# Performance work log

Measured on AMD Instinct MI355X. Metric: run time of the kernel, lower is better.

## Reference

```python
import jax, jax.numpy as jnp
import numpy as np

# ---- Haar DWT (levels=1, mode='zero'), matches pytorch_wavelets ordering ----
# For even H,W and filter length 2, zero-pad haar analysis reduces to
# non-overlapping 2x2 blocks. Subband order after the two 1D analyses
# (width first, then height): LL, (w-lo,h-hi), (w-hi,h-lo), HH.

def haar_dwt(x):
    a = x[..., 0::2, 0::2]
    b = x[..., 0::2, 1::2]
    c = x[..., 1::2, 0::2]
    d = x[..., 1::2, 1::2]
    ll = (a + b + c + d) * 0.5
    h0 = (a + b - c - d) * 0.5   # lo-width, hi-height
    h1 = (a - b + c - d) * 0.5   # hi-width, lo-height
    hh = (a - b - c + d) * 0.5
    return ll, jnp.stack([h0, h1, hh], axis=2)  # yh: (b,c,3,h/2,w/2)


def _interleave(u, v, axis):
    # interleave two equal-shaped arrays along `axis` (negative axis)
    s = list(u.shape)
    s[axis] *= 2
    return jnp.stack([u, v], axis=axis + len(u.shape) + 1).reshape(s)


def haar_idwt(ll, yh):
    h0, h1, hh = yh[:, :, 0], yh[:, :, 1], yh[:, :, 2]
    a = (ll + h0 + h1 + hh) * 0.5
    b = (ll + h0 - h1 - hh) * 0.5
    c = (ll - h0 + h1 - hh) * 0.5
    d = (ll - h0 - h1 + hh) * 0.5
    top = _interleave(a, b, -1)   # even rows
    bot = _interleave(c, d, -1)   # odd rows
    return _interleave(top, bot, -2)


def batched_dynamic_conv(feat, kernels, pad):
    """feat: (b,cin,h,w), kernels: (b,cout,cin,kh,kw) -> (b,cout,h,w).
    Per-sample kernels via grouped conv (batch as groups)."""
    bsz, cin, h, w = feat.shape
    cout, kh, kw = kernels.shape[1], kernels.shape[3], kernels.shape[4]
    lhs = feat.reshape(1, bsz * cin, h, w)
    rhs = kernels.reshape(bsz * cout, cin, kh, kw)
    out = jax.lax.conv_general_dilated(
        lhs, rhs, window_strides=(1, 1), padding=[(pad, pad), (pad, pad)],
        dimension_numbers=('NCHW', 'OIHW', 'NCHW'), feature_group_count=bsz)
    return out.reshape(bsz, cout, h, w)


def _dyn_conv_subband(feat, sub_kernels, attn_w, attn_b, pad=1):
    # attention: 1x1 conv -> global avg pool -> softmax over kernel_num
    logits = jnp.einsum('bchw,kc->bk', feat, attn_w) / (feat.shape[-2] * feat.shape[-1]) + attn_b
    att = jax.nn.softmax(logits, axis=1)                       # (b,K)
    kernels = jnp.einsum('bk,koiuv->boiuv', att, sub_kernels)  # (b,cout,cin,kh,kw)
    return batched_dynamic_conv(feat, kernels, pad)


def setup_inputs() -> dict:
    key = jax.random.key(0)
    k1, k2, k3, k4 = jax.random.split(key, 4)
    B, C, H, W = 8, 64, 128, 128
    K, SUB, COUT, KS = 4, 4, 64, 3  # kernel_num, 1+3*levels, out_channels, kernel_size
    return {
        'x': jax.random.normal(k1, (B, C, H, W), dtype=jnp.float32),
        'wt_kernels': jax.random.normal(k2, (K, SUB, COUT, C, KS, KS), dtype=jnp.float32) * 0.02,
        'attn_w': jax.random.normal(k3, (K, C), dtype=jnp.float32) * 0.1,
        'attn_b': jnp.zeros((K,), dtype=jnp.float32),
    }


def reference(x, wt_kernels, attn_w, attn_b):
    ll, yh = haar_dwt(x)
    subbands = [ll, yh[:, :, 0], yh[:, :, 1], yh[:, :, 2]]
    outs = [_dyn_conv_subband(sb, wt_kernels[:, i], attn_w, attn_b, pad=1)
            for i, sb in enumerate(subbands)]
    rec_yh = jnp.stack(outs[1:4], axis=2)  # (b,cout,3,h/2,w/2)
    return haar_idwt(outs[0], rec_yh)
```

## Files before the change

kernel.cpp:

```cpp
#include <hip/hip_runtime.h>
#include <hip/hip_bf16.h>
#include <math.h>


typedef __bf16 bf16x8 __attribute__((ext_vector_type(8)));
typedef float f32x4 __attribute__((ext_vector_type(4)));

__device__ __forceinline__ bf16x8 as_bf16x8(uint4 u) {
    union { uint4 a; bf16x8 b; } c; c.a = u; return c.b;
}
__device__ __forceinline__ unsigned short bf16bits(float f) {
    __hip_bfloat16 h = __float2bfloat16(f);
    union { __hip_bfloat16 h; unsigned short u; } c; c.h = h; return c.u;
}
__device__ __forceinline__ void gload_lds16(const uint4* g, uint4* l) {
    __builtin_amdgcn_global_load_lds(
        (const __attribute__((address_space(1))) unsigned int*)g,
        (__attribute__((address_space(3))) unsigned int*)l, 16, 0, 0);
}

#define FPLANE 34848
#define FROW   528

__global__ __launch_bounds__(256)
void dwt_kernel(const float* __restrict__ x, const float* __restrict__ attn_w,
                unsigned short* __restrict__ feats, float* __restrict__ plog) {
    __shared__ uint4 sT[2304];
    __shared__ float sred[64][4];
    unsigned short* sTu = (unsigned short*)sT;
    int y = blockIdx.x, b = blockIdx.y;
    int t = threadIdx.x;
    int c = t >> 2, q = t & 3;

    const float4* r0 = (const float4*)x + ((size_t)(b * 64 + c) * 128 + 2 * y) * 32;
    const float4* r1 = r0 + 32;

    float s0 = 0.f, s1 = 0.f, s2 = 0.f, s3 = 0.f;
    #pragma unroll
    for (int i = 0; i < 8; ++i) {
        int f = i * 4 + q;
        float4 p = r0[f], qq = r1[f];
        int xo = 2 * f;
        {
            float a = p.x, bb = p.y, cc = qq.x, dd = qq.y;
            float ll = (a + bb + cc + dd) * 0.5f, h0 = (a + bb - cc - dd) * 0.5f;
            float h1 = (a - bb + cc - dd) * 0.5f, hh = (a - bb - cc + dd) * 0.5f;
            s0 += ll; s1 += h0; s2 += h1; s3 += hh;
            sTu[0 * 4608 + xo * 72 + c] = bf16bits(ll);
            sTu[1 * 4608 + xo * 72 + c] = bf16bits(h0);
            sTu[2 * 4608 + xo * 72 + c] = bf16bits(h1);
            sTu[3 * 4608 + xo * 72 + c] = bf16bits(hh);
        }
        {
            float a = p.z, bb = p.w, cc = qq.z, dd = qq.w;
            float ll = (a + bb + cc + dd) * 0.5f, h0 = (a + bb - cc - dd) * 0.5f;
            float h1 = (a - bb + cc - dd) * 0.5f, hh = (a - bb - cc + dd) * 0.5f;
            s0 += ll; s1 += h0; s2 += h1; s3 += hh;
            sTu[0 * 4608 + (xo + 1) * 72 + c] = bf16bits(ll);
            sTu[1 * 4608 + (xo + 1) * 72 + c] = bf16bits(h0);
            sTu[2 * 4608 + (xo + 1) * 72 + c] = bf16bits(h1);
            sTu[3 * 4608 + (xo + 1) * 72 + c] = bf16bits(hh);
        }
    }
    s0 += __shfl_xor(s0, 1); s0 += __shfl_xor(s0, 2);
    s1 += __shfl_xor(s1, 1); s1 += __shfl_xor(s1, 2);
    s2 += __shfl_xor(s2, 1); s2 += __shfl_xor(s2, 2);
    s3 += __shfl_xor(s3, 1); s3 += __shfl_xor(s3, 2);
    if (q == 0) { sred[c][0] = s0; sred[c][1] = s1; sred[c][2] = s2; sred[c][3] = s3; }
    __syncthreads();
    if (t < 16) {
        int sub = t >> 2, k = t & 3;
        float acc = 0.f;
        #pragma unroll 8
        for (int cc = 0; cc < 64; ++cc)
            acc += attn_w[k * 64 + cc] * sred[cc][sub];
        plog[((size_t)(b * 4 + sub) * 4 + k) * 64 + y] = acc;
    }
    uint4* fpad = (uint4*)feats;
    const uint4 zz = make_uint4(0u, 0u, 0u, 0u);
    for (int e = t; e < 2112; e += 256) {
        int s = e / 528, r = e - s * 528;
        int px = r >> 3, ck = r & 7;
        uint4 v = zz;
        if (px >= 1 && px <= 64) v = sT[s * 576 + (px - 1) * 9 + ck];
        fpad[((size_t)(b * 4 + s) * 66 + (y + 1)) * FROW + r] = v;
    }
    if (y == 0) {
        for (int e = t; e < 2112; e += 256) {
            int s = e / 528, r = e - s * 528;
            fpad[(size_t)(b * 4 + s) * 66 * FROW + r] = zz;
        }
    } else if (y == 63) {
        for (int e = t; e < 2112; e += 256) {
            int s = e / 528, r = e - s * 528;
            fpad[((size_t)(b * 4 + s) * 66 + 65) * FROW + r] = zz;
        }
    }
}

__global__ __launch_bounds__(256)
void mix_kernel(const float* __restrict__ wt, const float* __restrict__ attn_b,
                const float* __restrict__ plog, unsigned short* __restrict__ wmix) {
    __shared__ float sLw[4][576];
    __shared__ float satt[8][4];
    int co = blockIdx.x, sub = blockIdx.y;
    int t = threadIdx.x;

    if (t < 32) {
        int b = t >> 2, k = t & 3;
        const float* pp = plog + ((size_t)(b * 4 + sub) * 4 + k) * 64;
        float acc = 0.f;
        #pragma unroll 8
        for (int yy = 0; yy < 64; ++yy) acc += pp[yy];
        float logit = acc * (1.0f / 4096.0f) + attn_b[k];
        float m = fmaxf(logit, __shfl_xor(logit, 1));
        m = fmaxf(m, __shfl_xor(m, 2));
        float e = expf(logit - m);
        float s = e + __shfl_xor(e, 1);
        s += __shfl_xor(s, 2);
        satt[b][k] = e / s;
    }
    for (int e = t; e < 2304; e += 256) {
        int k = e / 576, r = e - k * 576;
        sLw[k][r] = wt[((size_t)(k * 4 + sub) * 64 + co) * 576 + r];
    }
    __syncthreads();
    #pragma unroll
    for (int j = 0; j < 18; ++j) {
        int idx = j * 256 + t;
        int b = idx / 576;
        int r = idx - b * 576;
        int tap = r >> 6, ci = r & 63;
        int wi = ci * 9 + tap;
        float v = satt[b][0] * sLw[0][wi] + satt[b][1] * sLw[1][wi]
                + satt[b][2] * sLw[2][wi] + satt[b][3] * sLw[3][wi];
        wmix[((size_t)(b * 4 + sub) * 9 + tap) * 4096 + co * 64 + ci] = bf16bits(v);
    }
}

__global__ __launch_bounds__(256, 4)
void conv_kernel(const unsigned short* __restrict__ feats,
                 const unsigned short* __restrict__ wmix,
                 unsigned short* __restrict__ conv_out) {
    __shared__ uint4 sA[1296];
    __shared__ uint4 sW[1152];
    int bx = blockIdx.x;
    int tile = bx & 15, cg = bx >> 4;
    int sub = blockIdx.y, b = blockIdx.z;
    int y0 = (tile >> 2) * 16, x0 = (tile & 3) * 16;
    int t = threadIdx.x, w = t >> 6, l = t & 63;
    int l16 = l & 15, kg = l >> 4;
    int w4 = w * 4;
    const uint4* fp  = (const uint4*)feats + (size_t)(b * 4 + sub) * FPLANE;
    const uint4* wch = (const uint4*)wmix + (size_t)(b * 4 + sub) * 4608;

    f32x4 acc[4][2];
    #pragma unroll
    for (int r = 0; r < 4; ++r) {
        acc[r][0] = (f32x4){0.f, 0.f, 0.f, 0.f};
        acc[r][1] = (f32x4){0.f, 0.f, 0.f, 0.f};
    }

    #pragma unroll
    for (int ck8 = 0; ck8 < 8; ck8 += 4) {
        __syncthreads();
        #pragma unroll
        for (int i = 0; i < 5; ++i) {
            int e = t + i * 256;
            int py = e / 72, rr = e - py * 72, px = rr >> 2, g = rr & 3;
            gload_lds16(fp + (size_t)((y0 + py) * 66 + x0 + px) * 8 + ck8 + g, &sA[e]);
        }
        if (t < 16) {
            int e = 1280 + t;
            int rr = e - 1224, px = rr >> 2, g = rr & 3;
            sA[e] = fp[(size_t)((y0 + 17) * 66 + x0 + px) * 8 + ck8 + g];
        }
        #pragma unroll
        for (int i = 0; i < 4; ++i) {
            int e = t + i * 256;
            int tap = e >> 7, rr = e & 127, co = rr >> 2, g = rr & 3;
            gload_lds16(wch + tap * 512 + (cg * 32 + co) * 8 + ck8 + g, &sW[e]);
        }
        if (t < 128) {
            int e = 1024 + t;
            int tap = e >> 7, rr = e & 127, co = rr >> 2, g = rr & 3;
            gload_lds16(wch + tap * 512 + (cg * 32 + co) * 8 + ck8 + g, &sW[e]);
        }
        __syncthreads();
        uint4 af[4][3];
        #pragma unroll
        for (int i = 0; i < 4; ++i)
            #pragma unroll
            for (int dx = 0; dx < 3; ++dx)
                af[i][dx] = sA[((w4 + i) * 18 + l16 + dx) * 4 + kg];
        #pragma unroll
        for (int dy = 0; dy < 3; ++dy) {
            if (dy > 0) {
                #pragma unroll
                for (int i = 0; i < 3; ++i)
                    #pragma unroll
                    for (int dx = 0; dx < 3; ++dx)
                        af[i][dx] = af[i + 1][dx];
                #pragma unroll
                for (int dx = 0; dx < 3; ++dx)
                    af[3][dx] = sA[((w4 + dy + 3) * 18 + l16 + dx) * 4 + kg];
            }
            #pragma unroll
            for (int dx = 0; dx < 3; ++dx) {
                int tap = dy * 3 + dx;
                bf16x8 bw0 = as_bf16x8(sW[tap * 128 + l16 * 4 + kg]);
                bf16x8 bw1 = as_bf16x8(sW[tap * 128 + (16 + l16) * 4 + kg]);
                #pragma unroll
                for (int r = 0; r < 4; ++r) {
                    acc[r][0] = __builtin_amdgcn_mfma_f32_16x16x32_bf16(
                        as_bf16x8(af[r][dx]), bw0, acc[r][0], 0, 0, 0);
                    acc[r][1] = __builtin_amdgcn_mfma_f32_16x16x32_bf16(
                        as_bf16x8(af[r][dx]), bw1, acc[r][1], 0, 0, 0);
                }
            }
        }
    }
    size_t obase = (size_t)(b * 4 + sub) * 262144;
    #pragma unroll
    for (int r = 0; r < 4; ++r) {
        int yy = y0 + w4 + r;
        #pragma unroll
        for (int nn = 0; nn < 2; ++nn) {
            int co = cg * 32 + nn * 16 + l16;
            #pragma unroll
            for (int j = 0; j < 4; ++j) {
                int xx = x0 + kg * 4 + j;
                conv_out[obase + ((size_t)yy * 64 + xx) * 64 + co] = bf16bits(acc[r][nn][j]);
            }
        }
    }
}

__global__ __launch_bounds__(256)
void idwt_kernel(const unsigned short* __restrict__ conv_out,
                 float* __restrict__ out) {
    __shared__ uint4 sT[2304];
    int y = blockIdx.x, b = blockIdx.y;
    int t = threadIdx.x;
    const uint4* cch = (const uint4*)conv_out;
    for (int e = t; e < 2048; e += 256) {
        int s = e >> 9, xx = (e >> 3) & 63, ck = e & 7;
        sT[s * 576 + xx * 9 + ck] = cch[(size_t)(b * 4 + s) * 32768 + y * 512 + xx * 8 + ck];
    }
    __syncthreads();
    int xx = t & 63, cw = t >> 6;
    #pragma unroll
    for (int half = 0; half < 2; ++half) {
        int ckk = half * 4 + cw;
        bf16x8 v0 = as_bf16x8(sT[0 * 576 + xx * 9 + ckk]);
        bf16x8 v1 = as_bf16x8(sT[1 * 576 + xx * 9 + ckk]);
        bf16x8 v2 = as_bf16x8(sT[2 * 576 + xx * 9 + ckk]);
        bf16x8 v3 = as_bf16x8(sT[3 * 576 + xx * 9 + ckk]);
        #pragma unroll
        for (int j = 0; j < 8; ++j) {
            int c = ckk * 8 + j;
            float ll = (float)v0[j], h0 = (float)v1[j];
            float h1 = (float)v2[j], hh = (float)v3[j];
            float a = (ll + h0 + h1 + hh) * 0.5f;
            float bb = (ll + h0 - h1 - hh) * 0.5f;
            float cc = (ll - h0 + h1 - hh) * 0.5f;
            float dd = (ll - h0 - h1 + hh) * 0.5f;
            float2* o0 = (float2*)out + ((size_t)(b * 64 + c) * 128 + 2 * y) * 64 + xx;
            o0[0]  = make_float2(a, bb);
            o0[64] = make_float2(cc, dd);
        }
    }
}

extern "C" void kernel_launch(void* const* d_in, const int* in_sizes, int n_in,
                              void* d_out, int out_size, void* d_ws, size_t ws_size,
                              hipStream_t stream) {
    const float* x  = (const float*)d_in[0];
    const float* wt = (const float*)d_in[1];
    const float* aw = (const float*)d_in[2];
    const float* ab = (const float*)d_in[3];
    float* out = (float*)d_out;
    char* ws = (char*)d_ws;

    float* plog              = (float*)ws;
    unsigned short* feats    = (unsigned short*)(ws + 32768);
    unsigned short* wmix     = (unsigned short*)(ws + 32768 + 17842176);
    unsigned short* conv_out = (unsigned short*)(ws + 32768 + 17842176 + 2359296);

    hipLaunchKernelGGL(dwt_kernel, dim3(64, 8), dim3(256), 0, stream, x, aw, feats, plog);
    hipLaunchKernelGGL(mix_kernel, dim3(64, 4), dim3(256), 0, stream, wt, ab, plog, wmix);
    hipLaunchKernelGGL(conv_kernel, dim3(32, 4, 8), dim3(256), 0, stream,
                       feats, wmix, conv_out);
    hipLaunchKernelGGL(idwt_kernel, dim3(64, 8), dim3(256), 0, stream, conv_out, out);
}
```

Baseline: 121.2 us.

## Fuse subband convolutions with inverse Haar transform in one kernel

Merges the conv and idwt kernels: each block now loops over all four subbands, double-buffers the LDS staging of features and mixed weights, and folds each subband's conv result into four output-quadrant accumulators with signs. The inverse DWT is then written straight to the fp32 output with float4 stores. This removes the bf16 conv_out round trip through global memory and one kernel launch, and overlaps loads with MFMA work. In exchange, the grid shrinks from 1024 blocks of 256 threads to 256 blocks of 512 threads, and each thread holds more accumulator registers, which may reduce occupancy and parallelism.

```diff
diff --git a/kernel.cpp b/kernel.cpp
--- a/kernel.cpp
+++ b/kernel.cpp
@@ -138,136 +138,149 @@
     }
 }
 
-__global__ __launch_bounds__(256, 4)
-void conv_kernel(const unsigned short* __restrict__ feats,
-                 const unsigned short* __restrict__ wmix,
-                 unsigned short* __restrict__ conv_out) {
-    __shared__ uint4 sA[1296];
-    __shared__ uint4 sW[1152];
+__device__ __forceinline__ void stage_phase(const uint4* __restrict__ fp,
+                                            const uint4* __restrict__ wch,
+                                            uint4* sAb, uint4* sWb,
+                                            int y0, int x0, int cg, int ck8, int t) {
+    #pragma unroll
+    for (int i = 0; i < 2; ++i) {
+        int e = t + i * 512;
+        int py = e / 72, rr = e - py * 72, px = rr >> 2, g = rr & 3;
+        gload_lds16(fp + (size_t)((y0 + py) * 66 + x0 + px) * 8 + ck8 + g, &sAb[e]);
+    }
+    if (t < 256) {
+        int e = 1024 + t;
+        int py = e / 72, rr = e - py * 72, px = rr >> 2, g = rr & 3;
+        gload_lds16(fp + (size_t)((y0 + py) * 66 + x0 + px) * 8 + ck8 + g, &sAb[e]);
+    }
+    if (t < 16) {
+        int e = 1280 + t;
+        int rr = e - 1224, px = rr >> 2, g = rr & 3;
+        sAb[e] = fp[(size_t)((y0 + 17) * 66 + x0 + px) * 8 + ck8 + g];
+    }
+    #pragma unroll
+    for (int i = 0; i < 2; ++i) {
+        int e = t + i * 512;
+        int tap = e >> 7, rr = e & 127, co = rr >> 2, g = rr & 3;
+        gload_lds16(wch + tap * 512 + (cg * 32 + co) * 8 + ck8 + g, &sWb[e]);
+    }
+    if (t < 128) {
+        int e = 1024 + t;
+        int tap = e >> 7, rr = e & 127, co = rr >> 2, g = rr & 3;
+        gload_lds16(wch + tap * 512 + (cg * 32 + co) * 8 + ck8 + g, &sWb[e]);
+    }
+}
+
+__global__ __launch_bounds__(512)
+void conv_idwt_kernel(const unsigned short* __restrict__ feats,
+                      const unsigned short* __restrict__ wmix,
+                      float* __restrict__ out) {
+    __shared__ uint4 sA[2][1296];
+    __shared__ uint4 sW[2][1152];
     int bx = blockIdx.x;
     int tile = bx & 15, cg = bx >> 4;
-    int sub = blockIdx.y, b = blockIdx.z;
+    int b = blockIdx.y;
     int y0 = (tile >> 2) * 16, x0 = (tile & 3) * 16;
     int t = threadIdx.x, w = t >> 6, l = t & 63;
     int l16 = l & 15, kg = l >> 4;
-    int w4 = w * 4;
-    const uint4* fp  = (const uint4*)feats + (size_t)(b * 4 + sub) * FPLANE;
-    const uint4* wch = (const uint4*)wmix + (size_t)(b * 4 + sub) * 4608;
-
-    f32x4 acc[4][2];
-    #pragma unroll
-    for (int r = 0; r < 4; ++r) {
-        acc[r][0] = (f32x4){0.f, 0.f, 0.f, 0.f};
-        acc[r][1] = (f32x4){0.f, 0.f, 0.f, 0.f};
-    }
-
-    #pragma unroll
-    for (int ck8 = 0; ck8 < 8; ck8 += 4) {
-        __syncthreads();
+    int wy4 = (w >> 1) * 4, wn = w & 1;
+
+    const uint4* fpb = (const uint4*)feats + (size_t)b * 4 * FPLANE;
+    const uint4* wcb = (const uint4*)wmix + (size_t)b * 4 * 4608;
+
+    f32x4 accQ[4][4];
+    f32x4 accS[4];
+    #pragma unroll
+    for (int qd = 0; qd < 4; ++qd)
         #pragma unroll
-        for (int i = 0; i < 5; ++i) {
-            int e = t + i * 256;
-            int py = e / 72, rr = e - py * 72, px = rr >> 2, g = rr & 3;
-            gload_lds16(fp + (size_t)((y0 + py) * 66 + x0 + px) * 8 + ck8 + g, &sA[e]);
-        }
-        if (t < 16) {
-            int e = 1280 + t;
-            int rr = e - 1224, px = rr >> 2, g = rr & 3;
-            sA[e] = fp[(size_t)((y0 + 17) * 66 + x0 + px) * 8 + ck8 + g];
-        }
-        #pragma unroll
-        for (int i = 0; i < 4; ++i) {
-            int e = t + i * 256;
-            int tap = e >> 7, rr = e & 127, co = rr >> 2, g = rr & 3;
-            gload_lds16(wch + tap * 512 + (cg * 32 + co) * 8 + ck8 + g, &sW[e]);
-        }
-        if (t < 128) {
-            int e = 1024 + t;
-            int tap = e >> 7, rr = e & 127, co = rr >> 2, g = rr & 3;
-            gload_lds16(wch + tap * 512 + (cg * 32 + co) * 8 + ck8 + g, &sW[e]);
-        }
-        __syncthreads();
-        uint4 af[4][3];
-        #pragma unroll
-        for (int i = 0; i < 4; ++i)
+        for (int r = 0; r < 4; ++r)
+            accQ[qd][r] = (f32x4){0.f, 0.f, 0.f, 0.f};
+    #pragma unroll
+    for (int r = 0; r < 4; ++r) accS[r] = (f32x4){0.f, 0.f, 0.f, 0.f};
+
+    stage_phase(fpb, wcb, sA[0], sW[0], y0, x0, cg, 0, t);
+    __syncthreads();
+
+    #pragma unroll
+    for (int p = 0; p < 8; ++p) {
+        const int sub = p >> 1;
+        if (p < 7) {
+            const int ns = (p + 1) >> 1, nc = ((p + 1) & 1) * 4;
+            stage_phase(fpb + (size_t)ns * FPLANE, wcb + (size_t)ns * 4608,
+                        sA[(p + 1) & 1], sW[(p + 1) & 1], y0, x0, cg, nc, t);
+        }
+        {
+            const uint4* A = sA[p & 1];
+            const uint4* W = sW[p & 1];
+            uint4 af[4][3];
             #pragma unroll
-            for (int dx = 0; dx < 3; ++dx)
-                af[i][dx] = sA[((w4 + i) * 18 + l16 + dx) * 4 + kg];
-        #pragma unroll
-        for (int dy = 0; dy < 3; ++dy) {
-            if (dy > 0) {
+            for (int i = 0; i < 4; ++i)
                 #pragma unroll
-                for (int i = 0; i < 3; ++i)
+                for (int dx = 0; dx < 3; ++dx)
+                    af[i][dx] = A[((wy4 + i) * 18 + l16 + dx) * 4 + kg];
+            #pragma unroll
+            for (int dy = 0; dy < 3; ++dy) {
+                if (dy > 0) {
+                    #pragma unroll
+                    for (int i = 0; i < 3; ++i)
+                        #pragma unroll
+                        for (int dx = 0; dx < 3; ++dx)
+                            af[i][dx] = af[i + 1][dx];
                     #pragma unroll
                     for (int dx = 0; dx < 3; ++dx)
-                        af[i][dx] = af[i + 1][dx];
+                        af[3][dx] = A[((wy4 + dy + 3) * 18 + l16 + dx) * 4 + kg];
+                }
                 #pragma unroll
-                for (int dx = 0; dx < 3; ++dx)
-                    af[3][dx] = sA[((w4 + dy + 3) * 18 + l16 + dx) * 4 + kg];
-            }
-            #pragma unroll
-            for (int dx = 0; dx < 3; ++dx) {
-                int tap = dy * 3 + dx;
-                bf16x8 bw0 = as_bf16x8(sW[tap * 128 + l16 * 4 + kg]);
-                bf16x8 bw1 = as_bf16x8(sW[tap * 128 + (16 + l16) * 4 + kg]);
-                #pragma unroll
-                for (int r = 0; r < 4; ++r) {
-                    acc[r][0] = __builtin_amdgcn_mfma_f32_16x16x32_bf16(
-                        as_bf16x8(af[r][dx]), bw0, acc[r][0], 0, 0, 0);
-                    acc[r][1] = __builtin_amdgcn_mfma_f32_16x16x32_bf16(
-                        as_bf16x8(af[r][dx]), bw1, acc[r][1], 0, 0, 0);
+                for (int dx = 0; dx < 3; ++dx) {
+                    int tap = dy * 3 + dx;
+                    bf16x8 bw = as_bf16x8(W[tap * 128 + (wn * 16 + l16) * 4 + kg]);
+                    #pragma unroll
+                    for (int r = 0; r < 4; ++r)
+                        accS[r] = __builtin_amdgcn_mfma_f32_16x16x32_bf16(
+                            as_bf16x8(af[r][dx]), bw, accS[r], 0, 0, 0);
                 }
             }
         }
-    }
-    size_t obase = (size_t)(b * 4 + sub) * 262144;
+        if (p & 1) {
+            const float g1 = (sub <= 1) ? 1.f : -1.f;
+            const float g2 = (sub == 0 || sub == 2) ? 1.f : -1.f;
+            const float g3 = (sub == 0 || sub == 3) ? 1.f : -1.f;
+            #pragma unroll
+            for (int r = 0; r < 4; ++r) {
+                #pragma unroll
+                for (int j = 0; j < 4; ++j) {
+                    float v = accS[r][j];
+                    accQ[0][r][j] += v;
+                    accQ[1][r][j] += g1 * v;
+                    accQ[2][r][j] += g2 * v;
+                    accQ[3][r][j] += g3 * v;
+                    accS[r][j] = 0.f;
+                }
+            }
+        }
+        __syncthreads();
+    }
+
     #pragma unroll
     for (int r = 0; r < 4; ++r) {
-        int yy = y0 + w4 + r;
+        int y = y0 + wy4 + r;
+        int co = cg * 32 + wn * 16 + l16;
+        float* otop = out + ((size_t)(b * 64 + co) * 128 + 2 * y) * 128
+                          + 2 * (x0 + kg * 4);
+        float* obot = otop + 128;
         #pragma unroll
-        for (int nn = 0; nn < 2; ++nn) {
-            int co = cg * 32 + nn * 16 + l16;
-            #pragma unroll
-            for (int j = 0; j < 4; ++j) {
-                int xx = x0 + kg * 4 + j;
-                conv_out[obase + ((size_t)yy * 64 + xx) * 64 + co] = bf16bits(acc[r][nn][j]);
-            }
-        }
-    }
-}
-
-__global__ __launch_bounds__(256)
-void idwt_kernel(const unsigned short* __restrict__ conv_out,
-                 float* __restrict__ out) {
-    __shared__ uint4 sT[2304];
-    int y = blockIdx.x, b = blockIdx.y;
-    int t = threadIdx.x;
-    const uint4* cch = (const uint4*)conv_out;
-    for (int e = t; e < 2048; e += 256) {
-        int s = e >> 9, xx = (e >> 3) & 63, ck = e & 7;
-        sT[s * 576 + xx * 9 + ck] = cch[(size_t)(b * 4 + s) * 32768 + y * 512 + xx * 8 + ck];
-    }
-    __syncthreads();
-    int xx = t & 63, cw = t >> 6;
-    #pragma unroll
-    for (int half = 0; half < 2; ++half) {
-        int ckk = half * 4 + cw;
-        bf16x8 v0 = as_bf16x8(sT[0 * 576 + xx * 9 + ckk]);
-        bf16x8 v1 = as_bf16x8(sT[1 * 576 + xx * 9 + ckk]);
-        bf16x8 v2 = as_bf16x8(sT[2 * 576 + xx * 9 + ckk]);
-        bf16x8 v3 = as_bf16x8(sT[3 * 576 + xx * 9 + ckk]);
-        #pragma unroll
-        for (int j = 0; j < 8; ++j) {
-            int c = ckk * 8 + j;
-            float ll = (float)v0[j], h0 = (float)v1[j];
-            float h1 = (float)v2[j], hh = (float)v3[j];
-            float a = (ll + h0 + h1 + hh) * 0.5f;
-            float bb = (ll + h0 - h1 - hh) * 0.5f;
-            float cc = (ll - h0 + h1 - hh) * 0.5f;
-            float dd = (ll - h0 - h1 + hh) * 0.5f;
-            float2* o0 = (float2*)out + ((size_t)(b * 64 + c) * 128 + 2 * y) * 64 + xx;
-            o0[0]  = make_float2(a, bb);
-            o0[64] = make_float2(cc, dd);
+        for (int jp = 0; jp < 2; ++jp) {
+            float4 vt, vb;
+            vt.x = 0.5f * accQ[0][r][2 * jp];
+            vt.y = 0.5f * accQ[1][r][2 * jp];
+            vt.z = 0.5f * accQ[0][r][2 * jp + 1];
+            vt.w = 0.5f * accQ[1][r][2 * jp + 1];
+            vb.x = 0.5f * accQ[2][r][2 * jp];
+            vb.y = 0.5f * accQ[3][r][2 * jp];
+            vb.z = 0.5f * accQ[2][r][2 * jp + 1];
+            vb.w = 0.5f * accQ[3][r][2 * jp + 1];
+            *(float4*)(otop + 4 * jp) = vt;
+            *(float4*)(obot + 4 * jp) = vb;
         }
     }
 }
@@ -282,14 +295,12 @@
     float* out = (float*)d_out;
     char* ws = (char*)d_ws;
 
-    float* plog              = (float*)ws;
-    unsigned short* feats    = (unsigned short*)(ws + 32768);
-    unsigned short* wmix     = (unsigned short*)(ws + 32768 + 17842176);
-    unsigned short* conv_out = (unsigned short*)(ws + 32768 + 17842176 + 2359296);
+    float* plog           = (float*)ws;
+    unsigned short* feats = (unsigned short*)(ws + 32768);
+    unsigned short* wmix  = (unsigned short*)(ws + 32768 + 17842176);
 
     hipLaunchKernelGGL(dwt_kernel, dim3(64, 8), dim3(256), 0, stream, x, aw, feats, plog);
     hipLaunchKernelGGL(mix_kernel, dim3(64, 4), dim3(256), 0, stream, wt, ab, plog, wmix);
-    hipLaunchKernelGGL(conv_kernel, dim3(32, 4, 8), dim3(256), 0, stream,
-                       feats, wmix, conv_out);
-    hipLaunchKernelGGL(idwt_kernel, dim3(64, 8), dim3(256), 0, stream, conv_out, out);
-}
+    hipLaunchKernelGGL(conv_idwt_kernel, dim3(32, 8), dim3(512), 0, stream,
+                       feats, wmix, out);
+}
```

New measurement: 119.2 us. No clear change (-1.7%).
